# Kernel optimization log

Hardware: AMD Instinct MI355X
Metric: run time of the kernel (lower is better)

The kernel has to match this reference:

```python
import jax, jax.numpy as jnp
import numpy as np
from jax import lax

DIM = 512
DIM_KEY = 128


def _conv3x3_s2(x, w):
    # x: [N, C, H, W], w: [O, I, 3, 3]; stride-2, VALID (matches nn.Conv2d(dim, dim, 3, stride=2))
    return lax.conv_general_dilated(
        x, w, window_strides=(2, 2), padding='VALID',
        dimension_numbers=('NCHW', 'OIHW', 'NCHW'))


def setup_inputs() -> dict:
    key = jax.random.key(0)
    k1, k2, k3, k4, k5 = jax.random.split(key, 5)
    b, k, n, H, W = 8, 5, 5, 41, 41
    return {
        'img_query': jax.random.normal(k1, (b, DIM, H, W), dtype=jnp.float32),
        'img_supports': jax.random.normal(k2, (b, k, n, DIM, H, W), dtype=jnp.float32),
        'w_qk': jax.random.normal(k3, (DIM_KEY, DIM), dtype=jnp.float32) * 0.02,
        'w_v': jax.random.normal(k4, (DIM_KEY, DIM), dtype=jnp.float32) * 0.02,
        'w_ms': jax.random.normal(k5, (DIM, DIM, 3, 3), dtype=jnp.float32) * 0.02,
    }


def reference(img_query, img_supports, w_qk, w_v, w_ms):
    scale = DIM_KEY ** -0.5
    b, k, n = img_supports.shape[:3]

    # backbone `model` treated as identity; then multi-scale extracter (3x3 s2 conv)
    query_repr = _conv3x3_s2(img_query, w_ms)              # [b, c, h, w]
    h, w = query_repr.shape[-2:]
    supports = img_supports.reshape(b * k * n, DIM, *img_supports.shape[-2:])
    supports_repr = _conv3x3_s2(supports, w_ms)            # [bkn, c, h, w]

    # 1x1 convs as channel contractions
    query_q = jnp.einsum('bchw,dc->bdhw', query_repr, w_qk)
    query_v = jnp.einsum('bchw,dc->bdhw', query_repr, w_v)
    supports_k = jnp.einsum('schw,dc->sdhw', supports_repr, w_qk).reshape(b, k, n, DIM_KEY, h, w)
    supports_v = jnp.einsum('schw,dc->sdhw', supports_repr, w_v).reshape(b, k, n, DIM_KEY, h, w)

    # many-to-many cross attention over (n, i, j)
    sim = jnp.einsum('bchw,bkncij->bkhwnij', query_q, supports_k) * scale
    attn = jax.nn.softmax(sim.reshape(b, k, h, w, n * h * w), axis=-1)
    attn = attn.reshape(b, k, h, w, n, h, w)
    out = jnp.einsum('bkhwnij,bkncij->bkchw', attn, supports_v)

    out = out.reshape(b, k, -1)                     # [b, k, c*h*w]
    qv = query_v.reshape(b, 1, -1)                  # [b, 1, c*h*w]
    euclidean_dist = jnp.sum((qv - out) ** 2, axis=-1) / (h * w)
    return -euclidean_dist                          # [b, k]
```

## Files before the change

kernel.cpp:

```cpp
#include <hip/hip_runtime.h>

#define DIMC   512
#define HWIN   1681
#define WIN_   41
#define HWOUT  400
#define COUT   256
#define KD     4608
#define NIMG   208
#define NPAIR  40
#define NJ     2000
#define MTOT   83200

typedef __bf16 bf16;
typedef __bf16 bf16x4 __attribute__((ext_vector_type(4)));
typedef __bf16 bf16x8 __attribute__((ext_vector_type(8)));
typedef float  f32x16 __attribute__((ext_vector_type(16)));

#define OFF_WB   0ull
#define OFF_F    2359296ull
#define OFF_VT   44957696ull
#define OFF_DIST 65437696ull
#define OFF_R    65437952ull
#define WS_NEED  (OFF_R + 358039552ull)

__device__ __forceinline__ void gl2lds16(const void* g, void* l) {
  __builtin_amdgcn_global_load_lds((const __attribute__((address_space(1))) unsigned int*)g,
                                   (__attribute__((address_space(3))) unsigned int*)l,
                                   16, 0, 0);
}

__global__ __launch_bounds__(256) void k_wcomb(const float* __restrict__ wqk,
                                               const float* __restrict__ wv,
                                               const float* __restrict__ wms,
                                               bf16* __restrict__ Wb) {
  __shared__ float As[64][33];
  __shared__ float Bs[32][65];
  const int tid = threadIdx.x;
  const int bp = blockIdx.x, bn = blockIdx.y;
  const int tx = tid & 15, ty = tid >> 4;
  float acc[4][4] = {};
  for (int ko = 0; ko < 512; ko += 32) {
#pragma unroll
    for (int i = 0; i < 8; ++i) {
      int idx = tid + i * 256;
      int r = idx >> 5, c = idx & 31;
      int row = bn * 64 + r;
      As[r][c] = (row < 128) ? wqk[row * 512 + ko + c] : wv[(row - 128) * 512 + ko + c];
    }
#pragma unroll
    for (int i = 0; i < 8; ++i) {
      int idx = tid + i * 256;
      int r = idx >> 6, c = idx & 63;
      Bs[r][c] = wms[(size_t)(ko + r) * KD + bp * 64 + c];
    }
    __syncthreads();
#pragma unroll
    for (int kk = 0; kk < 32; ++kk) {
      float av[4], bv[4];
#pragma unroll
      for (int i = 0; i < 4; ++i) av[i] = As[ty * 4 + i][kk];
#pragma unroll
      for (int j = 0; j < 4; ++j) bv[j] = Bs[kk][tx * 4 + j];
#pragma unroll
      for (int i = 0; i < 4; ++i)
#pragma unroll
        for (int j = 0; j < 4; ++j) acc[i][j] += av[i] * bv[j];
    }
    __syncthreads();
  }
#pragma unroll
  for (int i = 0; i < 4; ++i)
#pragma unroll
    for (int j = 0; j < 4; ++j) {
      int n = bn * 64 + ty * 4 + i;
      int p = bp * 64 + tx * 4 + j;
      int c = p / 9, t = p - c * 9;
      Wb[(size_t)n * KD + t * DIMC + c] = (bf16)acc[i][j];
    }
}

__global__ __launch_bounds__(256) void k_repack(const float* __restrict__ q,
                                                const float* __restrict__ s,
                                                bf16* __restrict__ R) {
  __shared__ bf16 Ls[64][65];
  const int tid = threadIdx.x;
  const int bx = blockIdx.x, by = blockIdx.y, img = blockIdx.z;
  const float* src = (img < 8) ? (q + (size_t)img * DIMC * HWIN)
                               : (s + (size_t)(img - 8) * DIMC * HWIN);
  const int x0 = bx * 64, c0 = by * 64;
#pragma unroll
  for (int i = 0; i < 16; ++i) {
    int idx = i * 256 + tid;
    int r = idx >> 6, cx = idx & 63;
    int xx = x0 + cx;
    if (xx < HWIN) Ls[r][cx] = (bf16)src[(size_t)(c0 + r) * HWIN + xx];
  }
  __syncthreads();
#pragma unroll
  for (int i = 0; i < 4; ++i) {
    int idx = i * 256 + tid;
    int prow = idx >> 4, cq = idx & 15;
    int xx = x0 + prow;
    if (xx < HWIN) {
      bf16x4 v;
      v[0] = Ls[cq * 4 + 0][prow];
      v[1] = Ls[cq * 4 + 1][prow];
      v[2] = Ls[cq * 4 + 2][prow];
      v[3] = Ls[cq * 4 + 3][prow];
      *(bf16x4*)(R + ((size_t)img * HWIN + xx) * DIMC + c0 + cq * 4) = v;
    }
  }
}

__global__ __launch_bounds__(256, 2) void k_conv(const bf16* __restrict__ R,
                                                 const bf16* __restrict__ Wb,
                                                 bf16* __restrict__ F) {
  __shared__ __align__(16) bf16 As[128 * 64];
  __shared__ __align__(16) bf16 Bs[256 * 64];
  const int tid = threadIdx.x;
  const int lane = tid & 63, wave = tid >> 6;
  const int blk = blockIdx.x;

  unsigned aPix[4];
#pragma unroll
  for (int i = 0; i < 4; ++i) {
    int issue = wave * 4 + i;
    int m = issue * 8 + (lane >> 3);
    int g = (lane & 7) ^ (m & 7);
    int gm = blk * 128 + m;
    int img = gm / 400, p = gm - img * 400;
    int oy = p / 20, ox = p - oy * 20;
    aPix[i] = (unsigned)((img * HWIN + (2 * oy) * WIN_ + 2 * ox) * DIMC) + (unsigned)g * 8;
  }
  unsigned bOfs[8];
#pragma unroll
  for (int i = 0; i < 8; ++i) {
    int ib = wave * 8 + i;
    int n = ib * 8 + (lane >> 3);
    int g = (lane & 7) ^ (n & 7);
    bOfs[i] = (unsigned)n * KD + (unsigned)g * 8;
  }

  f32x16 acc[4][2];
#pragma unroll
  for (int mi = 0; mi < 4; ++mi)
#pragma unroll
    for (int ni = 0; ni < 2; ++ni)
#pragma unroll
      for (int r = 0; r < 16; ++r) acc[mi][ni][r] = 0.f;

  for (int t = 0; t < 9; ++t) {
    const int dy = t / 3, dx = t - dy * 3;
    const unsigned tapoff = (unsigned)((dy * WIN_ + dx) * DIMC);
    for (int cc = 0; cc < 8; ++cc) {
      const unsigned c0 = (unsigned)(cc * 64);
#pragma unroll
      for (int i = 0; i < 4; ++i) {
        int issue = wave * 4 + i;
        gl2lds16(R + aPix[i] + tapoff + c0, (char*)As + issue * 1024);
      }
#pragma unroll
      for (int i = 0; i < 8; ++i) {
        int ib = wave * 8 + i;
        gl2lds16(Wb + bOfs[i] + (unsigned)(t * DIMC) + c0, (char*)Bs + ib * 1024);
      }
      __syncthreads();
      const int mr = lane & 31;
#pragma unroll
      for (int kq = 0; kq < 4; ++kq) {
        const int chunk = kq * 2 + (lane >> 5);
        bf16x8 a[4], b[2];
#pragma unroll
        for (int mi = 0; mi < 4; ++mi) {
          int m = mi * 32 + mr;
          int slot = chunk ^ (m & 7);
          a[mi] = *(const bf16x8*)((const char*)As + m * 128 + slot * 16);
        }
#pragma unroll
        for (int ni = 0; ni < 2; ++ni) {
          int n = wave * 64 + ni * 32 + mr;
          int slot = chunk ^ (n & 7);
          b[ni] = *(const bf16x8*)((const char*)Bs + n * 128 + slot * 16);
        }
#pragma unroll
        for (int mi = 0; mi < 4; ++mi)
#pragma unroll
          for (int ni = 0; ni < 2; ++ni)
            acc[mi][ni] = __builtin_amdgcn_mfma_f32_32x32x16_bf16(a[mi], b[ni], acc[mi][ni], 0, 0, 0);
      }
      __syncthreads();
    }
  }
  const int col = lane & 31, hi = lane >> 5;
#pragma unroll
  for (int mi = 0; mi < 4; ++mi)
#pragma unroll
    for (int ni = 0; ni < 2; ++ni)
#pragma unroll
      for (int r = 0; r < 16; ++r) {
        int row = (r & 3) + 8 * (r >> 2) + 4 * hi;
        int gm = blk * 128 + mi * 32 + row;
        int ch = wave * 64 + ni * 32 + col;
        F[(size_t)gm * COUT + ch] = (bf16)acc[mi][ni][r];
      }
}

__global__ __launch_bounds__(256) void k_sim(const bf16* __restrict__ F,
                                             float* __restrict__ S) {
  __shared__ __align__(16) bf16 As[96 * 64];
  __shared__ __align__(16) bf16 Bs[256 * 64];
  const int tid = threadIdx.x, lane = tid & 63, wave = tid >> 6;
  const int mt = blockIdx.x, nt = blockIdx.y, pair = blockIdx.z;
  const int b = pair / 5, kidx = pair - b * 5;
  const int simg = 8 + b * 25 + kidx * 5;

  unsigned aBase[3];
#pragma unroll
  for (int i = 0; i < 3; ++i) {
    int issue = wave * 3 + i;
    int m = issue * 8 + (lane >> 3);
    int g = (lane & 7) ^ (m & 7);
    int pm = mt * 96 + m;
    if (pm >= HWOUT) pm = 0;
    aBase[i] = (unsigned)((b * HWOUT + pm) * COUT) + (unsigned)g * 8;
  }
  unsigned bBase[8];
#pragma unroll
  for (int i = 0; i < 8; ++i) {
    int ib = wave * 8 + i;
    int r = ib * 8 + (lane >> 3);
    int g = (lane & 7) ^ (r & 7);
    int jj = nt * 256 + r;
    if (jj >= NJ) jj = 0;
    int nimg = jj / HWOUT, ip = jj - nimg * HWOUT;
    bBase[i] = (unsigned)(((simg + nimg) * HWOUT + ip) * COUT) + (unsigned)g * 8;
  }

  f32x16 acc[3][2];
#pragma unroll
  for (int mi = 0; mi < 3; ++mi)
#pragma unroll
    for (int ni = 0; ni < 2; ++ni)
#pragma unroll
      for (int r = 0; r < 16; ++r) acc[mi][ni][r] = 0.f;

  for (int ks = 0; ks < 2; ++ks) {
    const int c0 = ks * 64;
#pragma unroll
    for (int i = 0; i < 3; ++i)
      gl2lds16(F + aBase[i] + c0, (char*)As + (wave * 3 + i) * 1024);
#pragma unroll
    for (int i = 0; i < 8; ++i)
      gl2lds16(F + bBase[i] + c0, (char*)Bs + (wave * 8 + i) * 1024);
    __syncthreads();
    const int mr = lane & 31;
#pragma unroll
    for (int kq = 0; kq < 4; ++kq) {
      const int chunk = kq * 2 + (lane >> 5);
      bf16x8 a[3], b[2];
#pragma unroll
      for (int mi = 0; mi < 3; ++mi) {
        int m = mi * 32 + mr;
        int slot = chunk ^ (m & 7);
        a[mi] = *(const bf16x8*)((const char*)As + m * 128 + slot * 16);
      }
#pragma unroll
      for (int ni = 0; ni < 2; ++ni) {
        int n = wave * 64 + ni * 32 + mr;
        int slot = chunk ^ (n & 7);
        b[ni] = *(const bf16x8*)((const char*)Bs + n * 128 + slot * 16);
      }
#pragma unroll
      for (int mi = 0; mi < 3; ++mi)
#pragma unroll
        for (int ni = 0; ni < 2; ++ni)
          acc[mi][ni] = __builtin_amdgcn_mfma_f32_32x32x16_bf16(a[mi], b[ni], acc[mi][ni], 0, 0, 0);
    }
    __syncthreads();
  }
  const float scale = 0.08838834764831845f;
  const int col = lane & 31, hi = lane >> 5;
#pragma unroll
  for (int mi = 0; mi < 3; ++mi)
#pragma unroll
    for (int ni = 0; ni < 2; ++ni)
#pragma unroll
      for (int r = 0; r < 16; ++r) {
        int row = (r & 3) + 8 * (r >> 2) + 4 * hi;
        int pix = mt * 96 + mi * 32 + row;
        int j = nt * 256 + wave * 64 + ni * 32 + col;
        if (pix < HWOUT && j < NJ)
          S[((size_t)pair * HWOUT + pix) * NJ + j] = acc[mi][ni][r] * scale;
      }
}

__global__ __launch_bounds__(256) void k_softmax(float* __restrict__ S) {
  const int row = blockIdx.x;
  const int tid = threadIdx.x;
  const int lane = tid & 63, wave = tid >> 6;
  float* rp = S + (size_t)row * NJ;
  float v[8];
  float mx = -1e30f;
#pragma unroll
  for (int i = 0; i < 8; ++i) {
    int idx = tid + i * 256;
    v[i] = (idx < NJ) ? rp[idx] : -1e30f;
    mx = fmaxf(mx, v[i]);
  }
  for (int off = 32; off > 0; off >>= 1) mx = fmaxf(mx, __shfl_xor(mx, off));
  __shared__ float sred[4];
  if (lane == 0) sred[wave] = mx;
  __syncthreads();
  mx = fmaxf(fmaxf(sred[0], sred[1]), fmaxf(sred[2], sred[3]));
  __syncthreads();
  float sum = 0.f;
#pragma unroll
  for (int i = 0; i < 8; ++i) {
    v[i] = __expf(v[i] - mx);
    sum += v[i];
  }
  for (int off = 32; off > 0; off >>= 1) sum += __shfl_xor(sum, off);
  if (lane == 0) sred[wave] = sum;
  __syncthreads();
  sum = sred[0] + sred[1] + sred[2] + sred[3];
  const float inv = 1.0f / sum;
  bf16* op = (bf16*)rp;
#pragma unroll
  for (int i = 0; i < 8; ++i) {
    int idx = tid + i * 256;
    if (idx < NJ) op[idx] = (bf16)(v[i] * inv);
  }
}

__global__ __launch_bounds__(256) void k_vt(const bf16* __restrict__ F,
                                            bf16* __restrict__ VT) {
  __shared__ bf16 Ls[64][132];
  const int tid = threadIdx.x;
  const int pt = blockIdx.x, n = blockIdx.y, pair = blockIdx.z;
  const int b = pair / 5, kidx = pair - b * 5;
  const int img = 8 + b * 25 + kidx * 5 + n;
#pragma unroll
  for (int i = 0; i < 8; ++i) {
    int idx = i * 256 + tid;
    int r = idx >> 5, cq = idx & 31;
    int ip = pt * 64 + r;
    if (ip < HWOUT) {
      bf16x4 t = *(const bf16x4*)(F + ((size_t)img * HWOUT + ip) * COUT + 128 + cq * 4);
      *(bf16x4*)(&Ls[r][cq * 4]) = t;
    }
  }
  __syncthreads();
#pragma unroll
  for (int i = 0; i < 8; ++i) {
    int idx = i * 256 + tid;
    int c = idx >> 4, iq = idx & 15;
    int ipb = pt * 64 + iq * 4;
    if (ipb + 3 < HWOUT) {
      bf16x4 v;
      v[0] = Ls[iq * 4 + 0][c];
      v[1] = Ls[iq * 4 + 1][c];
      v[2] = Ls[iq * 4 + 2][c];
      v[3] = Ls[iq * 4 + 3][c];
      *(bf16x4*)(VT + ((size_t)pair * 128 + c) * NJ + n * HWOUT + ipb) = v;
    }
  }
}

__global__ __launch_bounds__(256) void k_out(const char* __restrict__ Pbytes,
                                             const bf16* __restrict__ VT,
                                             const bf16* __restrict__ F,
                                             float* __restrict__ dist) {
  __shared__ __align__(16) bf16 As[96 * 128];
  __shared__ __align__(16) bf16 Bs[128 * 128];
  const int tid = threadIdx.x, lane = tid & 63, wave = tid >> 6;
  const int mt = blockIdx.x, pair = blockIdx.y;
  const int b = pair / 5;

  unsigned aByte[6]; int aGv[6];
#pragma unroll
  for (int i = 0; i < 6; ++i) {
    int issue = wave * 6 + i;
    int m = issue * 4 + (lane >> 4);
    int s_ = lane & 15;
    int g = s_ ^ (m & 7);
    int pm = mt * 96 + m;
    if (pm >= HWOUT) pm = 0;
    aByte[i] = (unsigned)((pair * HWOUT + pm) * 8000) + (unsigned)g * 16;
    aGv[i] = g;
  }
  unsigned bElem[8]; int bGv[8];
#pragma unroll
  for (int i = 0; i < 8; ++i) {
    int issue = wave * 8 + i;
    int c = issue * 4 + (lane >> 4);
    int s_ = lane & 15;
    int g = s_ ^ (c & 7);
    bElem[i] = (unsigned)((pair * 128 + c) * NJ) + (unsigned)g * 8;
    bGv[i] = g;
  }

  f32x16 acc[3];
#pragma unroll
  for (int mi = 0; mi < 3; ++mi)
#pragma unroll
    for (int r = 0; r < 16; ++r) acc[mi][r] = 0.f;

  const int mr = lane & 31;
  for (int step = 0; step < 16; ++step) {
    const int k0 = step * 128;
    const int nch = (step < 15) ? 16 : 10;
#pragma unroll
    for (int i = 0; i < 6; ++i) {
      if (aGv[i] < nch)
        gl2lds16(Pbytes + aByte[i] + k0 * 2, (char*)As + (wave * 6 + i) * 1024);
    }
#pragma unroll
    for (int i = 0; i < 8; ++i) {
      if (bGv[i] < nch)
        gl2lds16(VT + bElem[i] + k0, (char*)Bs + (wave * 8 + i) * 1024);
    }
    __syncthreads();
    auto body = [&](int kq) {
      const int chunk = kq * 2 + (lane >> 5);
      bf16x8 a[3], bb;
#pragma unroll
      for (int mi = 0; mi < 3; ++mi) {
        int m = mi * 32 + mr;
        int slot = chunk ^ (m & 7);
        a[mi] = *(const bf16x8*)((const char*)As + m * 256 + slot * 16);
      }
      {
        int n = wave * 32 + mr;
        int slot = chunk ^ (n & 7);
        bb = *(const bf16x8*)((const char*)Bs + n * 256 + slot * 16);
      }
#pragma unroll
      for (int mi = 0; mi < 3; ++mi)
        acc[mi] = __builtin_amdgcn_mfma_f32_32x32x16_bf16(a[mi], bb, acc[mi], 0, 0, 0);
    };
    if (step < 15) {
#pragma unroll
      for (int kq = 0; kq < 8; ++kq) body(kq);
    } else {
#pragma unroll
      for (int kq = 0; kq < 5; ++kq) body(kq);
    }
    __syncthreads();
  }

  const int col = lane & 31, hi = lane >> 5;
  float psum = 0.f;
#pragma unroll
  for (int mi = 0; mi < 3; ++mi)
#pragma unroll
    for (int r = 0; r < 16; ++r) {
      int row = (r & 3) + 8 * (r >> 2) + 4 * hi;
      int pix = mt * 96 + mi * 32 + row;
      if (pix < HWOUT) {
        int c = wave * 32 + col;
        float qv = (float)F[((size_t)b * HWOUT + pix) * COUT + 128 + c];
        float d = qv - acc[mi][r];
        psum += d * d;
      }
    }
  for (int off = 32; off > 0; off >>= 1) psum += __shfl_down(psum, off);
  __shared__ float ws4[4];
  if (lane == 0) ws4[wave] = psum;
  __syncthreads();
  if (tid == 0) atomicAdd(dist + pair, ws4[0] + ws4[1] + ws4[2] + ws4[3]);
}

__global__ void k_final(const float* __restrict__ dist, float* __restrict__ out) {
  int i = threadIdx.x;
  if (i < NPAIR) out[i] = -dist[i] * (1.0f / HWOUT);
}

extern "C" void kernel_launch(void* const* d_in, const int* in_sizes, int n_in,
                              void* d_out, int out_size, void* d_ws, size_t ws_size,
                              hipStream_t stream) {
  (void)in_sizes; (void)n_in; (void)out_size;
  if (ws_size < WS_NEED) return;

  const float* img_q = (const float*)d_in[0];
  const float* img_s = (const float*)d_in[1];
  const float* w_qk  = (const float*)d_in[2];
  const float* w_v   = (const float*)d_in[3];
  const float* w_ms  = (const float*)d_in[4];

  char* ws = (char*)d_ws;
  bf16*  Wb   = (bf16*)(ws + OFF_WB);
  bf16*  F    = (bf16*)(ws + OFF_F);
  bf16*  VT   = (bf16*)(ws + OFF_VT);
  float* dist = (float*)(ws + OFF_DIST);
  bf16*  R    = (bf16*)(ws + OFF_R);
  float* S    = (float*)(ws + OFF_R);

  hipMemsetAsync(dist, 0, NPAIR * sizeof(float), stream);
  k_wcomb  <<<dim3(72, 4),      256, 0, stream>>>(w_qk, w_v, w_ms, Wb);
  k_repack <<<dim3(27, 8, 208), 256, 0, stream>>>(img_q, img_s, R);
  k_conv   <<<dim3(650),        256, 0, stream>>>(R, Wb, F);
  k_sim    <<<dim3(5, 8, 40),   256, 0, stream>>>(F, S);
  k_softmax<<<dim3(16000),      256, 0, stream>>>(S);
  k_vt     <<<dim3(7, 5, 40),   256, 0, stream>>>(F, VT);
  k_out    <<<dim3(5, 40),      256, 0, stream>>>((const char*)S, VT, F, dist);
  k_final  <<<1, 64,             0, stream>>>(dist, (float*)d_out);
}
```

Baseline: 1.402 ms.

## Fuse softmax into output GEMM with online rescaling

Removes the separate softmax kernel and computes an online (flash-style) softmax inside k_out. Each step reads fp32 scores, tracks a running max and sum per row, writes bf16 probabilities into LDS, and rescales the accumulators before the MFMA step. The aim is to avoid a full extra read and write pass over the large score matrix and one kernel launch. In exchange, k_out has more per-step work: exps, a 64-float register array per thread, an extra sync point, and it now reads fp32 scores instead of bf16.

```diff
diff --git a/kernel.cpp b/kernel.cpp
--- a/kernel.cpp
+++ b/kernel.cpp
@@ -294,44 +294,6 @@
       }
 }
 
-__global__ __launch_bounds__(256) void k_softmax(float* __restrict__ S) {
-  const int row = blockIdx.x;
-  const int tid = threadIdx.x;
-  const int lane = tid & 63, wave = tid >> 6;
-  float* rp = S + (size_t)row * NJ;
-  float v[8];
-  float mx = -1e30f;
-#pragma unroll
-  for (int i = 0; i < 8; ++i) {
-    int idx = tid + i * 256;
-    v[i] = (idx < NJ) ? rp[idx] : -1e30f;
-    mx = fmaxf(mx, v[i]);
-  }
-  for (int off = 32; off > 0; off >>= 1) mx = fmaxf(mx, __shfl_xor(mx, off));
-  __shared__ float sred[4];
-  if (lane == 0) sred[wave] = mx;
-  __syncthreads();
-  mx = fmaxf(fmaxf(sred[0], sred[1]), fmaxf(sred[2], sred[3]));
-  __syncthreads();
-  float sum = 0.f;
-#pragma unroll
-  for (int i = 0; i < 8; ++i) {
-    v[i] = __expf(v[i] - mx);
-    sum += v[i];
-  }
-  for (int off = 32; off > 0; off >>= 1) sum += __shfl_xor(sum, off);
-  if (lane == 0) sred[wave] = sum;
-  __syncthreads();
-  sum = sred[0] + sred[1] + sred[2] + sred[3];
-  const float inv = 1.0f / sum;
-  bf16* op = (bf16*)rp;
-#pragma unroll
-  for (int i = 0; i < 8; ++i) {
-    int idx = tid + i * 256;
-    if (idx < NJ) op[idx] = (bf16)(v[i] * inv);
-  }
-}
-
 __global__ __launch_bounds__(256) void k_vt(const bf16* __restrict__ F,
                                             bf16* __restrict__ VT) {
   __shared__ bf16 Ls[64][132];
@@ -366,28 +328,17 @@
   }
 }
 
-__global__ __launch_bounds__(256) void k_out(const char* __restrict__ Pbytes,
-                                             const bf16* __restrict__ VT,
-                                             const bf16* __restrict__ F,
-                                             float* __restrict__ dist) {
+__global__ __launch_bounds__(256, 2) void k_out(const float* __restrict__ S,
+                                                const bf16* __restrict__ VT,
+                                                const bf16* __restrict__ F,
+                                                float* __restrict__ dist) {
   __shared__ __align__(16) bf16 As[96 * 128];
   __shared__ __align__(16) bf16 Bs[128 * 128];
+  __shared__ float mtab[96], ltab[96], fac[96];
   const int tid = threadIdx.x, lane = tid & 63, wave = tid >> 6;
   const int mt = blockIdx.x, pair = blockIdx.y;
   const int b = pair / 5;
 
-  unsigned aByte[6]; int aGv[6];
-#pragma unroll
-  for (int i = 0; i < 6; ++i) {
-    int issue = wave * 6 + i;
-    int m = issue * 4 + (lane >> 4);
-    int s_ = lane & 15;
-    int g = s_ ^ (m & 7);
-    int pm = mt * 96 + m;
-    if (pm >= HWOUT) pm = 0;
-    aByte[i] = (unsigned)((pair * HWOUT + pm) * 8000) + (unsigned)g * 16;
-    aGv[i] = g;
-  }
   unsigned bElem[8]; int bGv[8];
 #pragma unroll
   for (int i = 0; i < 8; ++i) {
@@ -399,27 +350,80 @@
     bGv[i] = g;
   }
 
+  const int sr = tid >> 1;
+  const int sh = tid & 1;
+  const bool srow_on = (sr < 96);
+  int pixr = mt * 96 + sr;
+  if (pixr >= HWOUT) pixr = 0;
+  const float* srow = S + (size_t)(pair * HWOUT + pixr) * NJ + sh * 64;
+
+  if (tid < 96) { mtab[tid] = -1e30f; ltab[tid] = 0.f; }
+
   f32x16 acc[3];
 #pragma unroll
   for (int mi = 0; mi < 3; ++mi)
 #pragma unroll
     for (int r = 0; r < 16; ++r) acc[mi][r] = 0.f;
 
+  __syncthreads();
   const int mr = lane & 31;
+
   for (int step = 0; step < 16; ++step) {
     const int k0 = step * 128;
     const int nch = (step < 15) ? 16 : 10;
 #pragma unroll
-    for (int i = 0; i < 6; ++i) {
-      if (aGv[i] < nch)
-        gl2lds16(Pbytes + aByte[i] + k0 * 2, (char*)As + (wave * 6 + i) * 1024);
-    }
-#pragma unroll
     for (int i = 0; i < 8; ++i) {
       if (bGv[i] < nch)
         gl2lds16(VT + bElem[i] + k0, (char*)Bs + (wave * 8 + i) * 1024);
     }
+    float p[64];
+    float m_new = -1e30f, fac_r = 1.0f;
+    if (srow_on) {
+      float rowmax = -1e30f;
+      const float* sp = srow + k0;
+#pragma unroll
+      for (int i = 0; i < 16; ++i) {
+        int jl = sh * 64 + i * 4;
+        float4 f;
+        if (k0 + jl < NJ) f = *(const float4*)(sp + i * 4);
+        else { f.x = -1e30f; f.y = -1e30f; f.z = -1e30f; f.w = -1e30f; }
+        p[i * 4 + 0] = f.x; p[i * 4 + 1] = f.y; p[i * 4 + 2] = f.z; p[i * 4 + 3] = f.w;
+        rowmax = fmaxf(rowmax, fmaxf(fmaxf(f.x, f.y), fmaxf(f.z, f.w)));
+      }
+      rowmax = fmaxf(rowmax, __shfl_xor(rowmax, 1));
+      float m_old = mtab[sr];
+      m_new = fmaxf(m_old, rowmax);
+      fac_r = __expf(m_old - m_new);
+      float psum = 0.f;
+#pragma unroll
+      for (int i = 0; i < 64; ++i) {
+        p[i] = __expf(p[i] - m_new);
+        psum += p[i];
+      }
+      psum += __shfl_xor(psum, 1);
+      if (sh == 0) {
+        mtab[sr] = m_new;
+        fac[sr] = fac_r;
+        ltab[sr] = ltab[sr] * fac_r + psum;
+      }
+#pragma unroll
+      for (int ci = 0; ci < 8; ++ci) {
+        bf16x8 w;
+#pragma unroll
+        for (int e = 0; e < 8; ++e) w[e] = (bf16)p[ci * 8 + e];
+        int chunk = sh * 8 + ci;
+        int slot = chunk ^ (sr & 7);
+        *(bf16x8*)((char*)As + sr * 256 + slot * 16) = w;
+      }
+    }
     __syncthreads();
+#pragma unroll
+    for (int mi = 0; mi < 3; ++mi)
+#pragma unroll
+      for (int r = 0; r < 16; ++r) {
+        int row = (r & 3) + 8 * (r >> 2) + 4 * (lane >> 5);
+        acc[mi][r] *= fac[mi * 32 + row];
+      }
     auto body = [&](int kq) {
       const int chunk = kq * 2 + (lane >> 5);
       bf16x8 a[3], bb;
@@ -457,9 +461,11 @@
       int row = (r & 3) + 8 * (r >> 2) + 4 * hi;
       int pix = mt * 96 + mi * 32 + row;
       if (pix < HWOUT) {
+        float l = ltab[mi * 32 + row];
+        float o = acc[mi][r] / l;
         int c = wave * 32 + col;
         float qv = (float)F[((size_t)b * HWOUT + pix) * COUT + 128 + c];
-        float d = qv - acc[mi][r];
+        float d = qv - o;
         psum += d * d;
       }
     }
@@ -500,8 +506,7 @@
   k_repack <<<dim3(27, 8, 208), 256, 0, stream>>>(img_q, img_s, R);
   k_conv   <<<dim3(650),        256, 0, stream>>>(R, Wb, F);
   k_sim    <<<dim3(5, 8, 40),   256, 0, stream>>>(F, S);
-  k_softmax<<<dim3(16000),      256, 0, stream>>>(S);
   k_vt     <<<dim3(7, 5, 40),   256, 0, stream>>>(F, VT);
-  k_out    <<<dim3(5, 40),      256, 0, stream>>>((const char*)S, VT, F, dist);
+  k_out    <<<dim3(5, 40),      256, 0, stream>>>(S, VT, F, dist);
   k_final  <<<1, 64,             0, stream>>>(dist, (float*)d_out);
 }
```

Result: no change. 1.402 ms (-0.1%).
